# Kernel optimization log

Measured on AMD Instinct MI355X. Metric: run time of the kernel, lower is better.

Reference implementation:

```python
import jax, jax.numpy as jnp
import numpy as np

B, S, D_MODEL, D_HEAD = 8, 2048, 1024, 128
MAX_ROUNDS = 3
THRESH = 0.1
SCALE = 1.0 / np.sqrt(float(D_HEAD))


def setup_inputs() -> dict:
    key = jax.random.key(0)
    ks = jax.random.split(key, 12)

    def lin(k, out_d, in_d):
        # torch Linear weight layout [out, in], y = x @ W.T + b
        return (jax.random.normal(k, (out_d, in_d), jnp.float32) / np.sqrt(float(in_d))).astype(jnp.float32)

    thesis_w = lin(ks[3], D_HEAD, D_HEAD)
    return {
        "x": jax.random.normal(ks[0], (B, S, D_MODEL), jnp.float32),
        "wq": lin(ks[1], D_HEAD, D_MODEL),
        "wk": lin(ks[2], D_HEAD, D_MODEL),
        "wv": lin(ks[4], D_HEAD, D_MODEL),
        "thesis_w": thesis_w,  # antithesis weight is -thesis_w per __init__
        "thesis_b": 0.02 * jax.random.normal(ks[5], (D_HEAD,), jnp.float32),
        "anti_b": 0.02 * jax.random.normal(ks[6], (D_HEAD,), jnp.float32),
        "s_w1": lin(ks[7], D_HEAD, 3 * D_HEAD),
        "s_b1": jnp.zeros((D_HEAD,), jnp.float32),
        "s_w2": lin(ks[8], D_HEAD, D_HEAD),
        "s_b2": jnp.zeros((D_HEAD,), jnp.float32),
        "g_w": lin(ks[9], 1, 2 * D_HEAD),
        "g_b": jnp.zeros((1,), jnp.float32),
    }


def reference(x, wq, wk, wv, thesis_w, thesis_b, anti_b, s_w1, s_b1, s_w2, s_b2, g_w, g_b):
    # q/k/v projections (no bias)
    q = jnp.einsum("bsm,hm->bsh", x, wq)
    k = jnp.einsum("bsm,hm->bsh", x, wk)
    v = jnp.einsum("bsm,hm->bsh", x, wv)

    attn = jax.nn.softmax(jnp.einsum("bqh,bkh->bqk", q, k) * SCALE, axis=-1)
    # dropout is identity at eval time
    cur = jnp.einsum("bqk,bkh->bqh", attn, v)  # [B,S,Dh]

    # attn_weights and v never change across rounds, so thesis/antithesis are
    # round-invariant: compute the context projections once.
    context = cur
    thesis = context @ thesis_w.T + thesis_b
    anti = context @ (-thesis_w).T + anti_b  # antithesis weight = -thesis weight

    active = jnp.ones((B, S), dtype=bool)
    for _ in range(MAX_ROUNDS):
        # emulate `if not active_mask.any(): break` under jit
        any_active = jnp.any(active)
        am = active[..., None].astype(x.dtype)
        at, aa, ac = thesis * am, anti * am, cur * am

        h = jax.nn.relu(jnp.concatenate([at, aa, ac], axis=-1) @ s_w1.T + s_b1)
        synth = h @ s_w2.T + s_b2
        gate = jax.nn.sigmoid(jnp.concatenate([ac, synth], axis=-1) @ g_w.T + g_b)
        update = gate * (synth - ac) * 0.1
        new = cur + update  # applied to ALL tokens, matching original

        stable = jnp.linalg.norm(update, axis=-1) < THRESH  # new - cur == update
        cur = jnp.where(any_active, new, cur)
        active = jnp.where(any_active, active & ~stable, active)
    return cur
```

## Files before the change

### kernel.cpp

```cpp
#include <hip/hip_runtime.h>
#include <hip/hip_bf16.h>

#define B_   8
#define S_   2048
#define DM   1024
#define DH   128
#define BS_  16384
#define SCALE_  0.08838834764831845f
#define SCALE2_ 0.12751744f

typedef unsigned short u16;
typedef unsigned int   u32;
typedef _Float16 half8 __attribute__((ext_vector_type(8)));
typedef __bf16   bf16x8 __attribute__((ext_vector_type(8)));
typedef float    f32x4 __attribute__((ext_vector_type(4)));
typedef u32      u32x4 __attribute__((ext_vector_type(4)));

union H8 { u32x4 v; u32 u[4]; half8 h; bf16x8 b; };

__device__ __forceinline__ float bf2f(u16 u) {
    union { u32 i; float f; } w; w.i = ((u32)u) << 16; return w.f;
}
__device__ __forceinline__ void unpack8(uint4 v, float* f) {
    f[0] = bf2f(v.x & 0xffff); f[1] = bf2f(v.x >> 16);
    f[2] = bf2f(v.y & 0xffff); f[3] = bf2f(v.y >> 16);
    f[4] = bf2f(v.z & 0xffff); f[5] = bf2f(v.z >> 16);
    f[6] = bf2f(v.w & 0xffff); f[7] = bf2f(v.w >> 16);
}
__device__ __forceinline__ float ldE(const void* b, size_t i, int isbf16) {
    return isbf16 ? bf2f(((const u16*)b)[i]) : ((const float*)b)[i];
}
__device__ __forceinline__ void ld8(const void* b, size_t i, int isbf16, float* f) {
    if (isbf16) {
        unpack8(*(const uint4*)((const u16*)b + i), f);
    } else {
        float4 a = *(const float4*)((const float*)b + i);
        float4 c = *(const float4*)((const float*)b + i + 4);
        f[0] = a.x; f[1] = a.y; f[2] = a.z; f[3] = a.w;
        f[4] = c.x; f[5] = c.y; f[6] = c.z; f[7] = c.w;
    }
}
__device__ __forceinline__ u32 f2pk(float v) {
    _Float16 h = (_Float16)v;
    _Float16 l = (_Float16)(v - (float)h);
    union { _Float16 f; u16 u; } a, b; a.f = h; b.f = l;
    return ((u32)a.u << 16) | (u32)b.u;
}
__device__ __forceinline__ void split8(const float* f, u32x4& hi, u32x4& lo) {
    u32 H[8], L[8];
#pragma unroll
    for (int j = 0; j < 8; ++j) {
        _Float16 h = (_Float16)f[j];
        _Float16 l = (_Float16)(f[j] - (float)h);
        union { _Float16 x; u16 u; } a, b; a.x = h; b.x = l;
        H[j] = a.u; L[j] = b.u;
    }
    hi = (u32x4){H[0] | (H[1] << 16), H[2] | (H[3] << 16), H[4] | (H[5] << 16), H[6] | (H[7] << 16)};
    lo = (u32x4){L[0] | (L[1] << 16), L[2] | (L[3] << 16), L[4] | (L[5] << 16), L[6] | (L[7] << 16)};
}
__device__ __forceinline__ u32 permHI(u32 eB, u32 eA) { return __builtin_amdgcn_perm(eB, eA, 0x07060302u); }
__device__ __forceinline__ u16 f2h(float v) { union { _Float16 f; u16 u; } a; a.f = (_Float16)v; return a.u; }
__device__ __forceinline__ float h2f(u16 u) { union { _Float16 f; u16 u; } a; a.u = u; return (float)a.f; }

__global__ void init_kernel(const void* x, int* flag, int* active, int* counts) {
    int i = blockIdx.x * 256 + threadIdx.x;
    if (i < BS_) active[i] = 1;
    if (i < 4) counts[i] = (i == 0) ? BS_ : 0;
    if (i == 0) {
        const u16* w = (const u16*)x;
        int sane = 0;
        for (int t = 0; t < 256; ++t) {
            int e = (w[2 * t] >> 7) & 0xFF;
            if (e >= 100 && e <= 135) ++sane;
        }
        *flag = (sane >= 192) ? 1 : 0;
    }
}

__global__ __launch_bounds__(256) void prepack_w_kernel(
    const void* __restrict__ wq, const void* __restrict__ wk, const void* __restrict__ wv,
    const int* __restrict__ flag, u32x4* __restrict__ wpk)
{
    const int isb = *flag;
    const int gid = blockIdx.x * 256 + threadIdx.x;
    const int l  = gid & 63;
    const int t  = (gid >> 6) & 7;
    const int ks = (gid >> 9) & 31;
    const int z  = gid >> 14;
    const void* W = (z == 0) ? wq : (z == 1) ? wk : wv;
    const int row = 16 * t + (l & 15);
    const int k0  = ks * 32 + 8 * (l >> 4);
    const size_t base = ((((size_t)z * 32 + ks) * 16) + 2 * t) * 64 + l;
    if (isb) {
        uint4 v = *(const uint4*)((const u16*)W + (size_t)row * DM + k0);
        wpk[base] = (u32x4){v.x, v.y, v.z, v.w};
    } else {
        float f[8];
        ld8(W, (size_t)row * DM + k0, 0, f);
        u32x4 hi, lo;
        split8(f, hi, lo);
        wpk[base]      = hi;
        wpk[base + 64] = lo;
    }
}

__global__ __launch_bounds__(256) void qkv_kernel(
    const void* __restrict__ x, const u32x4* __restrict__ wpk,
    const int* __restrict__ flag, u32* __restrict__ qout,
    u32x4* __restrict__ kfrag, u32x4* __restrict__ vfrag)
{
    const int isb = *flag;
    const int z = blockIdx.z;
    const int bx = blockIdx.x;
    const int m0 = ((bx & 7) * 32 + (bx >> 3)) * 64;
    const int tid = threadIdx.x;
    const int wave = tid >> 6, lane = tid & 63;
    const int qd = lane >> 4, c = lane & 15;

    __shared__ u32x4 WLraw[2][16][64];
    u32x4 (*WLb)[2][8][64] = (u32x4(*)[2][8][64])WLraw;
    u32x4 (*WLf)[8][2][64] = (u32x4(*)[8][2][64])WLraw;
    u16 (*TS)[136] = (u16(*)[136])WLraw;

    const u32x4* wz = wpk + (size_t)z * (32 * 16 * 64);
    const size_t arow = (size_t)(m0 + wave * 16 + c) * DM + 8 * qd;

#define STAGE2(i_, b_)                                                            \
    {                                                                             \
        _Pragma("unroll")                                                         \
        for (int _j = 0; _j < 4; ++_j) {                                          \
            const int _g = wave * 4 + _j, _ksub = _g >> 3, _t = _g & 7;           \
            __builtin_amdgcn_global_load_lds(                                     \
                (const __attribute__((address_space(1))) u32*)(                   \
                    wz + ((size_t)(2 * (i_) + _ksub) * 16 + 2 * _t) * 64 + lane), \
                (__attribute__((address_space(3))) u32*)&WLb[b_][_ksub][_t][0],   \
                16, 0, 0);                                                        \
        }                                                                         \
    }
#define STAGE_W(ks_, b_)                                                          \
    {                                                                             \
        const u32x4* _src = wz + ((size_t)(ks_) * 16 + 4 * wave) * 64 + lane;     \
        _Pragma("unroll")                                                         \
        for (int _j = 0; _j < 4; ++_j) {                                          \
            __builtin_amdgcn_global_load_lds(                                     \
                (const __attribute__((address_space(1))) u32*)(_src + _j * 64),   \
                (__attribute__((address_space(3))) u32*)&WLf[b_][2 * wave + (_j >> 1)][_j & 1][0], \
                16, 0, 0);                                                        \
        }                                                                         \
    }

    f32x4 acc[8] = {};

    if (isb) {
        const u16* xb = (const u16*)x;
        uint4 A0 = *(const uint4*)(xb + arow);
        uint4 A1 = *(const uint4*)(xb + arow + 32);
        STAGE2(0, 0);
        uint4 A0n = *(const uint4*)(xb + arow + 64);
        uint4 A1n = *(const uint4*)(xb + arow + 96);
        __syncthreads();
        for (int i = 0; i < 16; ++i) {
            const int cb = i & 1;
            if (i + 1 < 16) STAGE2(i + 1, cb ^ 1);
            H8 Ah0; Ah0.v = (u32x4){A0.x, A0.y, A0.z, A0.w};
            H8 Ah1; Ah1.v = (u32x4){A1.x, A1.y, A1.z, A1.w};
#pragma unroll
            for (int t = 0; t < 8; ++t) {
                H8 bh; bh.v = WLb[cb][0][t][lane];
                acc[t] = __builtin_amdgcn_mfma_f32_16x16x32_bf16(Ah0.b, bh.b, acc[t], 0, 0, 0);
            }
#pragma unroll
            for (int t = 0; t < 8; ++t) {
                H8 bh; bh.v = WLb[cb][1][t][lane];
                acc[t] = __builtin_amdgcn_mfma_f32_16x16x32_bf16(Ah1.b, bh.b, acc[t], 0, 0, 0);
            }
            A0 = A0n; A1 = A1n;
            if (i + 2 < 16) {
                A0n = *(const uint4*)(xb + arow + (size_t)(i + 2) * 64);
                A1n = *(const uint4*)(xb + arow + (size_t)(i + 2) * 64 + 32);
            }
            __syncthreads();
        }
    } else {
        float Ar[8], Arn[8];
        ld8(x, arow, 0, Ar);
        STAGE_W(0, 0);
        ld8(x, arow + 32, 0, Arn);
        __syncthreads();
        for (int ks = 0; ks < 32; ++ks) {
            const int cb = ks & 1;
            if (ks + 1 < 32) STAGE_W(ks + 1, cb ^ 1);
            H8 Ah, Al;
            split8(Ar, Ah.v, Al.v);
#pragma unroll
            for (int t = 0; t < 8; ++t) {
                H8 bh, bl;
                bh.v = WLf[cb][t][0][lane]; bl.v = WLf[cb][t][1][lane];
                acc[t] = __builtin_amdgcn_mfma_f32_16x16x32_f16(Al.h, bh.h, acc[t], 0, 0, 0);
                acc[t] = __builtin_amdgcn_mfma_f32_16x16x32_f16(Ah.h, bl.h, acc[t], 0, 0, 0);
                acc[t] = __builtin_amdgcn_mfma_f32_16x16x32_f16(Ah.h, bh.h, acc[t], 0, 0, 0);
            }
#pragma unroll
            for (int j = 0; j < 8; ++j) Ar[j] = Arn[j];
            if (ks + 2 < 32) ld8(x, arow + (size_t)(ks + 2) * 32, 0, Arn);
            __syncthreads();
        }
    }
#undef STAGE2
#undef STAGE_W

    if (z == 0) {
#pragma unroll
        for (int r = 0; r < 4; ++r) {
            const int row = m0 + wave * 16 + qd * 4 + r;
            u32* op = qout + (size_t)row * DH + c;
#pragma unroll
            for (int t = 0; t < 8; ++t) op[t * 16] = f2pk(acc[t][r]);
        }
    } else {
#pragma unroll
        for (int t = 0; t < 8; ++t)
#pragma unroll
            for (int r = 0; r < 4; ++r)
                TS[wave * 16 + qd * 4 + r][16 * t + c] = f2h(acc[t][r]);
        __syncthreads();
        if (z == 1) {
#pragma unroll
            for (int i = 0; i < 4; ++i) {
                const int f = tid + 256 * i;
                const int lf = f & 63, ks = (f >> 6) & 3, sub = f >> 8;
                const int key = sub * 16 + (lf & 15);
                const int d0  = ks * 32 + 8 * (lf >> 4);
                u32 w[4];
#pragma unroll
                for (int q = 0; q < 4; ++q)
                    w[q] = (u32)TS[key][d0 + 2 * q] | ((u32)TS[key][d0 + 2 * q + 1] << 16);
                kfrag[((size_t)(m0 / 16 + sub) * 4 + ks) * 64 + lf] = (u32x4){w[0], w[1], w[2], w[3]};
            }
        } else {
#pragma unroll
            for (int i = 0; i < 4; ++i) {
                const int f = tid + 256 * i;
                const int lf = f & 63, t = (f >> 6) & 7, sub = f >> 9;
                const int kb2 = sub * 32 + 8 * (lf >> 4);
                const int dh  = 16 * t + (lf & 15);
                u32 w[4];
#pragma unroll
                for (int q = 0; q < 4; ++q)
                    w[q] = (u32)TS[kb2 + 2 * q][dh] | ((u32)TS[kb2 + 2 * q + 1][dh] << 16);
                vfrag[((size_t)(m0 / 32 + sub) * 8 + t) * 64 + lf] = (u32x4){w[0], w[1], w[2], w[3]};
            }
        }
    }
}

template <bool WRITE_PARTIAL>
__device__ __forceinline__ void attn_body(
    const u32* qp, const u32x4* __restrict__ kfrag, const u32x4* __restrict__ vfrag,
    u16* outO, u16* outL, float* cur,
    int b, int q0, int kt0, int kt1, int part)
{
    const int tid = threadIdx.x;
    const int wave = tid >> 6, lane = tid & 63;
    const int qd = lane >> 4, c = lane & 15;

    __shared__ u16 PB[4][531];

    H8 Qh[4];
    {
        const u32* qr = qp + ((size_t)b * S_ + q0 + wave * 16 + c) * DH;
#pragma unroll
        for (int ks = 0; ks < 4; ++ks) {
            uint4 e0 = *(const uint4*)(qr + ks * 32 + qd * 8);
            uint4 e1 = *(const uint4*)(qr + ks * 32 + qd * 8 + 4);
            Qh[ks].u[0] = permHI(e0.y, e0.x); Qh[ks].u[1] = permHI(e0.w, e0.z);
            Qh[ks].u[2] = permHI(e1.y, e1.x); Qh[ks].u[3] = permHI(e1.w, e1.z);
        }
    }

    f32x4 O[8] = {};
    float lsum[4] = {};

    const u32x4* kb0 = kfrag + (size_t)b * 128 * 256;
    const u32x4* vb0 = vfrag + (size_t)b * 64 * 512;

    for (int kt = kt0; kt < kt1; ++kt) {
        const u32x4* kf = kb0 + (size_t)kt * 512;
        const u32x4* vf = vb0 + (size_t)kt * 512;

        f32x4 S0 = {}, S1 = {};
#pragma unroll
        for (int ks = 0; ks < 4; ++ks) {
            H8 kh;
            kh.v = kf[ks * 64 + lane];
            S0 = __builtin_amdgcn_mfma_f32_16x16x32_f16(Qh[ks].h, kh.h, S0, 0, 0, 0);
            kh.v = kf[256 + ks * 64 + lane];
            S1 = __builtin_amdgcn_mfma_f32_16x16x32_f16(Qh[ks].h, kh.h, S1, 0, 0, 0);
        }

        u16* pw = PB[wave];
#pragma unroll
        for (int r = 0; r < 4; ++r) {
            float e0 = exp2f(fmaf(S0[r], SCALE2_, -4.0f));
            float e1 = exp2f(fmaf(S1[r], SCALE2_, -4.0f));
            lsum[r] += e0 + e1;
            pw[(4 * qd + r) * 33 + c]      = f2h(e0);
            pw[(4 * qd + r) * 33 + 16 + c] = f2h(e1);
        }

        u16 e[8];
#pragma unroll
        for (int j = 0; j < 8; ++j) e[j] = pw[c * 33 + 8 * qd + j];
        H8 Ph;
        Ph.u[0] = (u32)e[0] | ((u32)e[1] << 16);
        Ph.u[1] = (u32)e[2] | ((u32)e[3] << 16);
        Ph.u[2] = (u32)e[4] | ((u32)e[5] << 16);
        Ph.u[3] = (u32)e[6] | ((u32)e[7] << 16);

#pragma unroll
        for (int t = 0; t < 8; ++t) {
            H8 vh;
            vh.v = vf[t * 64 + lane];
            O[t] = __builtin_amdgcn_mfma_f32_16x16x32_f16(Ph.h, vh.h, O[t], 0, 0, 0);
        }
    }

    if (WRITE_PARTIAL) {
        float lred[4];
#pragma unroll
        for (int r = 0; r < 4; ++r) {
            float l = lsum[r];
            l += __shfl_xor(l, 1); l += __shfl_xor(l, 2);
            l += __shfl_xor(l, 4); l += __shfl_xor(l, 8);
            lred[r] = l;
        }
        const size_t rb = (size_t)b * S_ + q0 + wave * 16 + 4 * qd;
        u16* Op = outO + (size_t)part * ((size_t)BS_ * DH);
#pragma unroll
        for (int t = 0; t < 8; ++t)
#pragma unroll
            for (int r = 0; r < 4; ++r)
                Op[(rb + r) * DH + t * 16 + c] = f2h(O[t][r]);
        if (c == 0) {
            u16* lp = outL + (size_t)part * BS_;
#pragma unroll
            for (int r = 0; r < 4; ++r) lp[rb + r] = f2h(lred[r]);
        }
    } else {
        float linv[4];
#pragma unroll
        for (int r = 0; r < 4; ++r) {
            float l = lsum[r];
            l += __shfl_xor(l, 1); l += __shfl_xor(l, 2);
            l += __shfl_xor(l, 4); l += __shfl_xor(l, 8);
            linv[r] = 1.0f / l;
        }
        const size_t rb = (size_t)b * S_ + q0 + wave * 16 + 4 * qd;
#pragma unroll
        for (int t = 0; t < 8; ++t)
#pragma unroll
            for (int r = 0; r < 4; ++r)
                cur[(rb + r) * DH + t * 16 + c] = O[t][r] * linv[r];
    }
}

__global__ __launch_bounds__(256) void attn_kernel(
    const u32* qp, const u32x4* __restrict__ kfrag, const u32x4* __restrict__ vfrag, float* cur)
{
    const int rid = blockIdx.x + 32 * blockIdx.y;
    attn_body<false>(qp, kfrag, vfrag, nullptr, nullptr, cur,
                     rid & 7, ((rid >> 3) & 31) * 64, 0, S_ / 32, 0);
}

__global__ __launch_bounds__(256) void attn_split_kernel(
    const u32* qp, const u32x4* __restrict__ kfrag, const u32x4* __restrict__ vfrag,
    u16* __restrict__ Opart, u16* __restrict__ lpart)
{
    const int rid = blockIdx.x + 32 * (blockIdx.y + 8 * blockIdx.z);
    const int b    = rid & 7;
    const int qx   = (rid >> 3) & 31;
    const int part = rid >> 8;
    const int quart = S_ / 128;
    attn_body<true>(qp, kfrag, vfrag, Opart, lpart, nullptr,
                    b, qx * 64, part * quart, (part + 1) * quart, part);
}

__global__ __launch_bounds__(256) void combine_kernel(
    const u16* __restrict__ Opart, const u16* __restrict__ lpart,
    float* __restrict__ cur)
{
    const size_t N1 = (size_t)BS_ * DH;
    const size_t i0 = ((size_t)blockIdx.x * 256 + threadIdx.x) * 16;
    const int row = (int)(i0 >> 7);
    const float lt = h2f(lpart[row]) + h2f(lpart[BS_ + row])
                   + h2f(lpart[2 * BS_ + row]) + h2f(lpart[3 * BS_ + row]);
    const float linv = 1.0f / lt;
    float acc[16] = {};
#pragma unroll
    for (int p = 0; p < 4; ++p) {
        const u16* op = Opart + (size_t)p * N1 + i0;
        uint4 v0 = *(const uint4*)op;
        uint4 v1 = *(const uint4*)(op + 8);
        const u32 w[8] = {v0.x, v0.y, v0.z, v0.w, v1.x, v1.y, v1.z, v1.w};
#pragma unroll
        for (int j = 0; j < 8; ++j) {
            acc[2 * j]     += h2f((u16)(w[j] & 0xffff));
            acc[2 * j + 1] += h2f((u16)(w[j] >> 16));
        }
    }
#pragma unroll
    for (int t = 0; t < 4; ++t)
        *(float4*)(cur + i0 + t * 4) = make_float4(
            acc[4*t] * linv, acc[4*t+1] * linv, acc[4*t+2] * linv, acc[4*t+3] * linv);
}

__global__ __launch_bounds__(256) void prepack_rw_kernel(
    const void* __restrict__ tw, const void* __restrict__ w1, const void* __restrict__ w2,
    const int* __restrict__ flag, u32x4* __restrict__ pk)
{
    const int isb = *flag;
    const int gid = blockIdx.x * 256 + threadIdx.x;
    const int l = gid & 63, t = (gid >> 6) & 7, ks = (gid >> 9) & 3, mat = gid >> 11;
    const int row = 16 * t + (l & 15);
    const int k0  = ks * 32 + 8 * (l >> 4);
    float f[8];
    if (mat == 0)      ld8(tw, (size_t)row * DH + k0, isb, f);
    else if (mat <= 3) ld8(w1, (size_t)row * 384 + (mat - 1) * 128 + k0, isb, f);
    else               ld8(w2, (size_t)row * DH + k0, isb, f);
    u32x4 hi, lo;
    split8(f, hi, lo);
    const size_t base = (((size_t)mat * 4 + ks) * 16 + 2 * t) * 64 + l;
    pk[base] = hi; pk[base + 64] = lo;
}

struct Afrag { H8 h[4], l[4]; };
__device__ __forceinline__ void splitA(const float (&A)[4][8], Afrag& F) {
#pragma unroll
    for (int ks = 0; ks < 4; ++ks) split8(A[ks], F.h[ks].v, F.l[ks].v);
}

__global__ __launch_bounds__(256) void round_kernel(
    const float* cur0, const float* curr,
    const u32x4* __restrict__ pk,
    const void* __restrict__ tb, const void* __restrict__ ab,
    const void* __restrict__ b1, const void* __restrict__ b2,
    const void* __restrict__ gw, const void* __restrict__ gb,
    const int* __restrict__ flag, int* active, int* counts, int r,
    float* cur_out, void* dout)
{
    const int isb = *flag;
    const int tok0 = blockIdx.x * 64;
    const int tid = threadIdx.x;
    const bool last = (dout != nullptr);

    if (counts[r] <= 0) {
        if (last) {
            for (int e = tid; e < 64 * DH; e += 256) {
                size_t idx = (size_t)tok0 * DH + e;
                float v = curr[idx];
                if (isb) ((__hip_bfloat16*)dout)[idx] = __float2bfloat16(v);
                else     ((float*)dout)[idx] = v;
            }
        }
        return;
    }

    const int wave = tid >> 6, lane = tid & 63;
    const int qd = lane >> 4, c = lane & 15;

    __shared__ u32x4 WB[4][8][64];
    __shared__ u16 T0S[64][132];
    __shared__ u16 HSS[64][132];
    __shared__ float actS[64], tbS[128], abS[128], b1S[128], b2S[128], gwS[256];
    __shared__ int blkcnt;

    auto stageB = [&](int mat) {
#pragma unroll
        for (int j = 0; j < 8; ++j) {
            __builtin_amdgcn_global_load_lds(
                (const __attribute__((address_space(1))) u32*)(
                    pk + (((size_t)mat * 4 + wave) * 16 + 2 * j) * 64 + lane),
                (__attribute__((address_space(3))) u32*)&WB[wave][j][0],
                16, 0, 0);
        }
    };
    auto stageF = [&](int mat, int h) {
#pragma unroll
        for (int j = 0; j < 8; ++j) {
            const int g = wave * 8 + j, kl = g >> 4, p = (g >> 3) & 1, t = g & 7;
            __builtin_amdgcn_global_load_lds(
                (const __attribute__((address_space(1))) u32*)(
                    pk + (((size_t)mat * 4 + 2 * h + kl) * 16 + 2 * t + p) * 64 + lane),
                (__attribute__((address_space(3))) u32*)&WB[kl * 2 + p][t][0],
                16, 0, 0);
        }
    };
    auto gemmB = [&](const Afrag& F, f32x4 (&acc)[8]) {
#pragma unroll
        for (int ks = 0; ks < 4; ++ks)
#pragma unroll
            for (int t = 0; t < 8; ++t) {
                H8 bh; bh.v = WB[ks][t][lane];
                acc[t] = __builtin_amdgcn_mfma_f32_16x16x32_f16(F.l[ks].h, bh.h, acc[t], 0, 0, 0);
                acc[t] = __builtin_amdgcn_mfma_f32_16x16x32_f16(F.h[ks].h, bh.h, acc[t], 0, 0, 0);
            }
    };
    auto gemmF = [&](const Afrag& F, int h, f32x4 (&acc)[8]) {
#pragma unroll
        for (int kl = 0; kl < 2; ++kl) {
            const int ks = 2 * h + kl;
#pragma unroll
            for (int t = 0; t < 8; ++t) {
                H8 bh, bl;
                bh.v = WB[kl * 2][t][lane];
                bl.v = WB[kl * 2 + 1][t][lane];
                acc[t] = __builtin_amdgcn_mfma_f32_16x16x32_f16(F.l[ks].h, bh.h, acc[t], 0, 0, 0);
                acc[t] = __builtin_amdgcn_mfma_f32_16x16x32_f16(F.h[ks].h, bl.h, acc[t], 0, 0, 0);
                acc[t] = __builtin_amdgcn_mfma_f32_16x16x32_f16(F.h[ks].h, bh.h, acc[t], 0, 0, 0);
            }
        }
    };
    auto runGemm = [&](int mat, const Afrag& F, f32x4 (&acc)[8]) {
        if (isb) {
            gemmB(F, acc);
        } else {
            gemmF(F, 0, acc);
            __syncthreads();
            stageF(mat, 1);
            __syncthreads();
            gemmF(F, 1, acc);
        }
    };

    if (isb) stageB(0); else stageF(0, 0);
    if (tid < 64) actS[tid] = active[tok0 + tid] ? 1.0f : 0.0f;
    if (tid < 128) {
        tbS[tid] = ldE(tb, tid, isb); abS[tid] = ldE(ab, tid, isb);
        b1S[tid] = ldE(b1, tid, isb); b2S[tid] = ldE(b2, tid, isb);
    }
    gwS[tid] = ldE(gw, tid, isb);
    if (tid == 0) blkcnt = 0;
    const float gbf = ldE(gb, 0, isb);

    const int rowl = 16 * wave + c;
    const int hr   = 16 * wave + 4 * qd;

    float A1[4][8];
    {
        const float* cr = cur0 + (size_t)(tok0 + rowl) * DH;
#pragma unroll
        for (int ks = 0; ks < 4; ++ks) {
            *(float4*)&A1[ks][0] = *(const float4*)(cr + ks * 32 + 8 * qd);
            *(float4*)&A1[ks][4] = *(const float4*)(cr + ks * 32 + 8 * qd + 4);
        }
    }
    Afrag FA; splitA(A1, FA);
    __syncthreads();

    {
        f32x4 acc[8] = {};
        runGemm(0, FA, acc);
#pragma unroll
        for (int t = 0; t < 8; ++t)
#pragma unroll
            for (int rr = 0; rr < 4; ++rr)
                T0S[hr + rr][16 * t + c] = f2h(acc[t][rr]);
    }
    __syncthreads();
    if (isb) stageB(1); else stageF(1, 0);

    f32x4 acc1[8] = {};
    const float am_r = actS[rowl];
    {
        float Ac[4][8];
#pragma unroll
        for (int ks = 0; ks < 4; ++ks)
#pragma unroll
            for (int j = 0; j < 8; ++j) {
                const int k = ks * 32 + 8 * qd + j;
                Ac[ks][j] = (h2f(T0S[rowl][k]) + tbS[k]) * am_r;
            }
        Afrag FC; splitA(Ac, FC);
        __syncthreads();
        runGemm(1, FC, acc1);
    }
    __syncthreads();
    if (isb) stageB(2); else stageF(2, 0);
    {
        float Ac[4][8];
#pragma unroll
        for (int ks = 0; ks < 4; ++ks)
#pragma unroll
            for (int j = 0; j < 8; ++j) {
                const int k = ks * 32 + 8 * qd + j;
                Ac[ks][j] = (abS[k] - h2f(T0S[rowl][k])) * am_r;
            }
        Afrag FC; splitA(Ac, FC);
        __syncthreads();
        runGemm(2, FC, acc1);
    }
    __syncthreads();
    if (isb) stageB(3); else stageF(3, 0);
    {
        float Ac[4][8];
        const float* cr = curr + (size_t)(tok0 + rowl) * DH;
#pragma unroll
        for (int ks = 0; ks < 4; ++ks) {
            float4 a0 = *(const float4*)(cr + ks * 32 + 8 * qd);
            float4 a1 = *(const float4*)(cr + ks * 32 + 8 * qd + 4);
            Ac[ks][0] = a0.x * am_r; Ac[ks][1] = a0.y * am_r;
            Ac[ks][2] = a0.z * am_r; Ac[ks][3] = a0.w * am_r;
            Ac[ks][4] = a1.x * am_r; Ac[ks][5] = a1.y * am_r;
            Ac[ks][6] = a1.z * am_r; Ac[ks][7] = a1.w * am_r;
        }
        Afrag FC; splitA(Ac, FC);
        __syncthreads();
        runGemm(3, FC, acc1);
    }
#pragma unroll
    for (int t = 0; t < 8; ++t)
#pragma unroll
        for (int rr = 0; rr < 4; ++rr)
            HSS[hr + rr][16 * t + c] = f2h(fmaxf(acc1[t][rr] + b1S[16 * t + c], 0.0f));
    __syncthreads();
    if (isb) stageB(4); else stageF(4, 0);
    {
        float Ac[4][8];
#pragma unroll
        for (int ks = 0; ks < 4; ++ks)
#pragma unroll
            for (int j = 0; j < 8; ++j)
                Ac[ks][j] = h2f(HSS[rowl][ks * 32 + 8 * qd + j]);
        Afrag FC; splitA(Ac, FC);
        __syncthreads();
        f32x4 acc2[8] = {};
        runGemm(4, FC, acc2);
#pragma unroll
        for (int t = 0; t < 8; ++t)
#pragma unroll
            for (int rr = 0; rr < 4; ++rr)
                T0S[hr + rr][16 * t + c] = f2h(acc2[t][rr] + b2S[16 * t + c]);
    }
    __syncthreads();

    const int tok = tid >> 2, d0 = (tid & 3) * 32;
    const float am = actS[tok];
    const float* cp = curr + (size_t)(tok0 + tok) * DH + d0;
    float cv[32];
#pragma unroll
    for (int t = 0; t < 8; ++t) {
        float4 vv = *(const float4*)(cp + t * 4);
        cv[t * 4] = vv.x; cv[t * 4 + 1] = vv.y; cv[t * 4 + 2] = vv.z; cv[t * 4 + 3] = vv.w;
    }
    float srow[32];
#pragma unroll
    for (int e = 0; e < 32; ++e) srow[e] = h2f(T0S[tok][d0 + e]);
    float gp = 0.0f;
#pragma unroll
    for (int e = 0; e < 32; ++e)
        gp += cv[e] * am * gwS[d0 + e] + srow[e] * gwS[128 + d0 + e];
    gp += __shfl_xor(gp, 1, 4);
    gp += __shfl_xor(gp, 2, 4);
    const float gate = 1.0f / (1.0f + __expf(-(gp + gbf)));
    float ss = 0.0f; float up[32];
#pragma unroll
    for (int e = 0; e < 32; ++e) {
        float u = gate * (srow[e] - cv[e] * am) * 0.1f;
        up[e] = u; ss += u * u;
    }
    ss += __shfl_xor(ss, 1, 4);
    ss += __shfl_xor(ss, 2, 4);
    const bool stable = sqrtf(ss) < 0.1f;

    if (last) {
        size_t off = (size_t)(tok0 + tok) * DH + d0;
        if (isb) {
            __hip_bfloat16* op = (__hip_bfloat16*)dout + off;
#pragma unroll
            for (int e = 0; e < 32; ++e) op[e] = __float2bfloat16(cv[e] + up[e]);
        } else {
            float* op = (float*)dout + off;
#pragma unroll
            for (int t = 0; t < 8; ++t)
                *(float4*)(op + t * 4) = make_float4(cv[t * 4] + up[t * 4], cv[t * 4 + 1] + up[t * 4 + 1],
                                                     cv[t * 4 + 2] + up[t * 4 + 2], cv[t * 4 + 3] + up[t * 4 + 3]);
        }
    } else {
        float* op = cur_out + (size_t)(tok0 + tok) * DH + d0;
#pragma unroll
        for (int t = 0; t < 8; ++t)
            *(float4*)(op + t * 4) = make_float4(cv[t * 4] + up[t * 4], cv[t * 4 + 1] + up[t * 4 + 1],
                                                 cv[t * 4 + 2] + up[t * 4 + 2], cv[t * 4 + 3] + up[t * 4 + 3]);
    }
    const int newact = (am > 0.0f && !stable) ? 1 : 0;
    if ((tid & 3) == 0) {
        active[tok0 + tok] = newact;
        if (newact) atomicAdd(&blkcnt, 1);
    }
    __syncthreads();
    if (tid == 0 && blkcnt > 0) atomicAdd(&counts[r + 1], blkcnt);
}

extern "C" void kernel_launch(void* const* d_in, const int* in_sizes, int n_in,
                              void* d_out, int out_size, void* d_ws, size_t ws_size,
                              hipStream_t stream) {
    const void* x  = d_in[0];
    const void* wq = d_in[1];
    const void* wk = d_in[2];
    const void* wv = d_in[3];
    const void* tw = d_in[4];
    const void* tb = d_in[5];
    const void* ab = d_in[6];
    const void* w1 = d_in[7];
    const void* b1 = d_in[8];
    const void* w2 = d_in[9];
    const void* b2 = d_in[10];
    const void* gw = d_in[11];
    const void* gb = d_in[12];

    u32* ws = (u32*)d_ws;
    const size_t N1 = (size_t)BS_ * DH;
    u32* qp = ws;
    u32* kp = ws + N1;
    u32* vp = ws + 2 * N1;
    int* active = (int*)(ws + 3 * N1);
    int* counts = active + BS_;
    int* flag   = counts + 4;
    float* cur0  = (float*)qp;
    float* cur_r = (float*)kp;
    u16* Opart16 = (u16*)(ws + 3 * N1 + 32768);
    u16* lpart16 = (u16*)(ws + 5 * N1 + 32768);
    const bool big_ws = ws_size >= (size_t)42300000;
    u32x4* wpk = (u32x4*)(ws + 3 * N1 + 32768);
    u32x4* pkRW = (u32x4*)vp;
    u32x4* kfragP = (u32x4*)kp;
    u32x4* vfragP = (u32x4*)vp;

    init_kernel<<<dim3(BS_ / 256), 256, 0, stream>>>(x, flag, active, counts);
    prepack_w_kernel<<<dim3(192), 256, 0, stream>>>(wq, wk, wv, flag, wpk);
    qkv_kernel<<<dim3(BS_ / 64, 1, 3), 256, 0, stream>>>(x, wpk, flag, qp, kfragP, vfragP);
    if (big_ws) {
        attn_split_kernel<<<dim3(S_ / 64, B_, 4), 256, 0, stream>>>(qp, kfragP, vfragP, Opart16, lpart16);
        combine_kernel<<<dim3(512), 256, 0, stream>>>(Opart16, lpart16, cur0);
    } else {
        attn_kernel<<<dim3(S_ / 64, B_), 256, 0, stream>>>(qp, kfragP, vfragP, cur0);
    }
    prepack_rw_kernel<<<dim3(40), 256, 0, stream>>>(tw, w1, w2, flag, pkRW);
    round_kernel<<<dim3(BS_ / 64), 256, 0, stream>>>(
        cur0, cur0, pkRW, tb, ab, b1, b2, gw, gb, flag, active, counts, 0, cur_r, nullptr);
    round_kernel<<<dim3(BS_ / 64), 256, 0, stream>>>(
        cur0, cur_r, pkRW, tb, ab, b1, b2, gw, gb, flag, active, counts, 1, cur_r, nullptr);
    round_kernel<<<dim3(BS_ / 64), 256, 0, stream>>>(
        cur0, cur_r, pkRW, tb, ab, b1, b2, gw, gb, flag, active, counts, 2, cur_r, d_out);
}
```

Measured before the change: 261.3 us.

## Halve round-kernel token tile, split N across waves, double-buffer weight staging

The round kernel now processes 32 tokens per block instead of 64, with waves arranged as 2 row groups by 2 column halves, so each wave computes 4 output tiles rather than 8. Weight staging into LDS is double-buffered, so the next matrix's load is issued before the current GEMM runs, and several barriers are removed. T0S and HSS are merged into one shared buffer. The aim is more blocks for better occupancy and to overlap weight fetches with MFMA work. In exchange, each weight matrix is fetched twice as often across the grid and per-block fixed overhead grows.

```diff
diff --git a/kernel.cpp b/kernel.cpp
--- a/kernel.cpp
+++ b/kernel.cpp
@@ -449,13 +449,13 @@
     float* cur_out, void* dout)
 {
     const int isb = *flag;
-    const int tok0 = blockIdx.x * 64;
+    const int tok0 = blockIdx.x * 32;
     const int tid = threadIdx.x;
     const bool last = (dout != nullptr);
 
     if (counts[r] <= 0) {
         if (last) {
-            for (int e = tid; e < 64 * DH; e += 256) {
+            for (int e = tid; e < 32 * DH; e += 256) {
                 size_t idx = (size_t)tok0 * DH + e;
                 float v = curr[idx];
                 if (isb) ((__hip_bfloat16*)dout)[idx] = __float2bfloat16(v);
@@ -467,73 +467,75 @@
 
     const int wave = tid >> 6, lane = tid & 63;
     const int qd = lane >> 4, c = lane & 15;
-
-    __shared__ u32x4 WB[4][8][64];
-    __shared__ u16 T0S[64][132];
-    __shared__ u16 HSS[64][132];
-    __shared__ float actS[64], tbS[128], abS[128], b1S[128], b2S[128], gwS[256];
+    const int rowg = wave >> 1, colh = wave & 1;
+
+    __shared__ u32x4 WB[2][4][8][64];
+    __shared__ u16 TS[32][132];
+    __shared__ float actS[32], tbS[128], abS[128], b1S[128], b2S[128], gwS[256];
     __shared__ int blkcnt;
 
-    auto stageB = [&](int mat) {
+    auto stageB = [&](int mat, int buf) {
 #pragma unroll
         for (int j = 0; j < 8; ++j) {
+            const int g = wave * 8 + j, ks = g >> 3, t = g & 7;
             __builtin_amdgcn_global_load_lds(
                 (const __attribute__((address_space(1))) u32*)(
-                    pk + (((size_t)mat * 4 + wave) * 16 + 2 * j) * 64 + lane),
-                (__attribute__((address_space(3))) u32*)&WB[wave][j][0],
+                    pk + (((size_t)mat * 4 + ks) * 16 + 2 * t) * 64 + lane),
+                (__attribute__((address_space(3))) u32*)&WB[buf][ks][t][0],
                 16, 0, 0);
         }
     };
-    auto stageF = [&](int mat, int h) {
+    auto stageF = [&](int mat, int h, int buf) {
 #pragma unroll
         for (int j = 0; j < 8; ++j) {
             const int g = wave * 8 + j, kl = g >> 4, p = (g >> 3) & 1, t = g & 7;
             __builtin_amdgcn_global_load_lds(
                 (const __attribute__((address_space(1))) u32*)(
                     pk + (((size_t)mat * 4 + 2 * h + kl) * 16 + 2 * t + p) * 64 + lane),
-                (__attribute__((address_space(3))) u32*)&WB[kl * 2 + p][t][0],
+                (__attribute__((address_space(3))) u32*)&WB[buf][kl * 2 + p][t][0],
                 16, 0, 0);
         }
     };
-    auto gemmB = [&](const Afrag& F, f32x4 (&acc)[8]) {
+    auto gemmB = [&](const Afrag& F, int buf, f32x4 (&acc)[4]) {
 #pragma unroll
         for (int ks = 0; ks < 4; ++ks)
 #pragma unroll
-            for (int t = 0; t < 8; ++t) {
-                H8 bh; bh.v = WB[ks][t][lane];
-                acc[t] = __builtin_amdgcn_mfma_f32_16x16x32_f16(F.l[ks].h, bh.h, acc[t], 0, 0, 0);
-                acc[t] = __builtin_amdgcn_mfma_f32_16x16x32_f16(F.h[ks].h, bh.h, acc[t], 0, 0, 0);
+            for (int tl = 0; tl < 4; ++tl) {
+                H8 bh; bh.v = WB[buf][ks][4 * colh + tl][lane];
+                acc[tl] = __builtin_amdgcn_mfma_f32_16x16x32_f16(F.l[ks].h, bh.h, acc[tl], 0, 0, 0);
+                acc[tl] = __builtin_amdgcn_mfma_f32_16x16x32_f16(F.h[ks].h, bh.h, acc[tl], 0, 0, 0);
             }
     };
-    auto gemmF = [&](const Afrag& F, int h, f32x4 (&acc)[8]) {
+    auto gemmFh = [&](const Afrag& F, int h, int buf, f32x4 (&acc)[4]) {
 #pragma unroll
         for (int kl = 0; kl < 2; ++kl) {
             const int ks = 2 * h + kl;
 #pragma unroll
-            for (int t = 0; t < 8; ++t) {
+            for (int tl = 0; tl < 4; ++tl) {
                 H8 bh, bl;
-                bh.v = WB[kl * 2][t][lane];
-                bl.v = WB[kl * 2 + 1][t][lane];
-                acc[t] = __builtin_amdgcn_mfma_f32_16x16x32_f16(F.l[ks].h, bh.h, acc[t], 0, 0, 0);
-                acc[t] = __builtin_amdgcn_mfma_f32_16x16x32_f16(F.h[ks].h, bl.h, acc[t], 0, 0, 0);
-                acc[t] = __builtin_amdgcn_mfma_f32_16x16x32_f16(F.h[ks].h, bh.h, acc[t], 0, 0, 0);
+                bh.v = WB[buf][kl * 2][4 * colh + tl][lane];
+                bl.v = WB[buf][kl * 2 + 1][4 * colh + tl][lane];
+                acc[tl] = __builtin_amdgcn_mfma_f32_16x16x32_f16(F.l[ks].h, bh.h, acc[tl], 0, 0, 0);
+                acc[tl] = __builtin_amdgcn_mfma_f32_16x16x32_f16(F.h[ks].h, bl.h, acc[tl], 0, 0, 0);
+                acc[tl] = __builtin_amdgcn_mfma_f32_16x16x32_f16(F.h[ks].h, bh.h, acc[tl], 0, 0, 0);
             }
         }
     };
-    auto runGemm = [&](int mat, const Afrag& F, f32x4 (&acc)[8]) {
+    auto STAGE = [&](int mat, int buf) { if (isb) stageB(mat, buf); else stageF(mat, 0, buf); };
+    auto GEMM = [&](int mat, const Afrag& F, int buf, f32x4 (&acc)[4]) {
         if (isb) {
-            gemmB(F, acc);
+            gemmB(F, buf, acc);
         } else {
-            gemmF(F, 0, acc);
+            gemmFh(F, 0, buf, acc);
             __syncthreads();
-            stageF(mat, 1);
+            stageF(mat, 1, buf);
             __syncthreads();
-            gemmF(F, 1, acc);
+            gemmFh(F, 1, buf, acc);
         }
     };
 
-    if (isb) stageB(0); else stageF(0, 0);
-    if (tid < 64) actS[tid] = active[tok0 + tid] ? 1.0f : 0.0f;
+    STAGE(0, 0);
+    if (tid < 32) actS[tid] = active[tok0 + tid] ? 1.0f : 0.0f;
     if (tid < 128) {
         tbS[tid] = ldE(tb, tid, isb); abS[tid] = ldE(ab, tid, isb);
         b1S[tid] = ldE(b1, tid, isb); b2S[tid] = ldE(b2, tid, isb);
@@ -542,8 +544,8 @@
     if (tid == 0) blkcnt = 0;
     const float gbf = ldE(gb, 0, isb);
 
-    const int rowl = 16 * wave + c;
-    const int hr   = 16 * wave + 4 * qd;
+    const int rowl = 16 * rowg + c;
+    const int hr   = 16 * rowg + 4 * qd;
 
     float A1[4][8];
     {
@@ -557,19 +559,20 @@
     Afrag FA; splitA(A1, FA);
     __syncthreads();
 
+    STAGE(1, 1);
     {
-        f32x4 acc[8] = {};
-        runGemm(0, FA, acc);
-#pragma unroll
-        for (int t = 0; t < 8; ++t)
+        f32x4 accT[4] = {};
+        GEMM(0, FA, 0, accT);
+#pragma unroll
+        for (int tl = 0; tl < 4; ++tl)
 #pragma unroll
             for (int rr = 0; rr < 4; ++rr)
-                T0S[hr + rr][16 * t + c] = f2h(acc[t][rr]);
+                TS[hr + rr][16 * (4 * colh + tl) + c] = f2h(accT[tl][rr]);
     }
     __syncthreads();
-    if (isb) stageB(1); else stageF(1, 0);
-
-    f32x4 acc1[8] = {};
+
+    STAGE(2, 0);
+    f32x4 acc1[4] = {};
     const float am_r = actS[rowl];
     {
         float Ac[4][8];
@@ -578,14 +581,14 @@
 #pragma unroll
             for (int j = 0; j < 8; ++j) {
                 const int k = ks * 32 + 8 * qd + j;
-                Ac[ks][j] = (h2f(T0S[rowl][k]) + tbS[k]) * am_r;
+                Ac[ks][j] = (h2f(TS[rowl][k]) + tbS[k]) * am_r;
             }
         Afrag FC; splitA(Ac, FC);
-        __syncthreads();
-        runGemm(1, FC, acc1);
+        GEMM(1, FC, 1, acc1);
     }
     __syncthreads();
-    if (isb) stageB(2); else stageF(2, 0);
+
+    STAGE(3, 1);
     {
         float Ac[4][8];
 #pragma unroll
@@ -593,14 +596,14 @@
 #pragma unroll
             for (int j = 0; j < 8; ++j) {
                 const int k = ks * 32 + 8 * qd + j;
-                Ac[ks][j] = (abS[k] - h2f(T0S[rowl][k])) * am_r;
+                Ac[ks][j] = (abS[k] - h2f(TS[rowl][k])) * am_r;
             }
         Afrag FC; splitA(Ac, FC);
-        __syncthreads();
-        runGemm(2, FC, acc1);
+        GEMM(2, FC, 0, acc1);
     }
     __syncthreads();
-    if (isb) stageB(3); else stageF(3, 0);
+
+    STAGE(4, 0);
     {
         float Ac[4][8];
         const float* cr = curr + (size_t)(tok0 + rowl) * DH;
@@ -614,62 +617,67 @@
             Ac[ks][6] = a1.z * am_r; Ac[ks][7] = a1.w * am_r;
         }
         Afrag FC; splitA(Ac, FC);
-        __syncthreads();
-        runGemm(3, FC, acc1);
-    }
-#pragma unroll
-    for (int t = 0; t < 8; ++t)
-#pragma unroll
-        for (int rr = 0; rr < 4; ++rr)
-            HSS[hr + rr][16 * t + c] = f2h(fmaxf(acc1[t][rr] + b1S[16 * t + c], 0.0f));
+        GEMM(3, FC, 1, acc1);
+    }
+#pragma unroll
+    for (int tl = 0; tl < 4; ++tl)
+#pragma unroll
+        for (int rr = 0; rr < 4; ++rr) {
+            const int col = 16 * (4 * colh + tl) + c;
+            TS[hr + rr][col] = f2h(fmaxf(acc1[tl][rr] + b1S[col], 0.0f));
+        }
     __syncthreads();
-    if (isb) stageB(4); else stageF(4, 0);
+
     {
         float Ac[4][8];
 #pragma unroll
         for (int ks = 0; ks < 4; ++ks)
 #pragma unroll
             for (int j = 0; j < 8; ++j)
-                Ac[ks][j] = h2f(HSS[rowl][ks * 32 + 8 * qd + j]);
+                Ac[ks][j] = h2f(TS[rowl][ks * 32 + 8 * qd + j]);
         Afrag FC; splitA(Ac, FC);
+        f32x4 acc2[4] = {};
+        GEMM(4, FC, 0, acc2);
         __syncthreads();
-        f32x4 acc2[8] = {};
-        runGemm(4, FC, acc2);
-#pragma unroll
-        for (int t = 0; t < 8; ++t)
-#pragma unroll
-            for (int rr = 0; rr < 4; ++rr)
-                T0S[hr + rr][16 * t + c] = f2h(acc2[t][rr] + b2S[16 * t + c]);
+#pragma unroll
+        for (int tl = 0; tl < 4; ++tl)
+#pragma unroll
+            for (int rr = 0; rr < 4; ++rr) {
+                const int col = 16 * (4 * colh + tl) + c;
+                TS[hr + rr][col] = f2h(acc2[tl][rr] + b2S[col]);
+            }
     }
     __syncthreads();
 
-    const int tok = tid >> 2, d0 = (tid & 3) * 32;
+    const int tok = tid >> 3, d0 = (tid & 7) * 16;
     const float am = actS[tok];
     const float* cp = curr + (size_t)(tok0 + tok) * DH + d0;
-    float cv[32];
-#pragma unroll
-    for (int t = 0; t < 8; ++t) {
+    float cv[16];
+#pragma unroll
+    for (int t = 0; t < 4; ++t) {
         float4 vv = *(const float4*)(cp + t * 4);
         cv[t * 4] = vv.x; cv[t * 4 + 1] = vv.y; cv[t * 4 + 2] = vv.z; cv[t * 4 + 3] = vv.w;
     }
-    float srow[32];
-#pragma unroll
-    for (int e = 0; e < 32; ++e) srow[e] = h2f(T0S[tok][d0 + e]);
+    float srow[16];
+#pragma unroll
+    for (int e = 0; e < 16; ++e) srow[e] = h2f(TS[tok][d0 + e]);
     float gp = 0.0f;
 #pragma unroll
-    for (int e = 0; e < 32; ++e)
+    for (int e = 0; e < 16; ++e)
         gp += cv[e] * am * gwS[d0 + e] + srow[e] * gwS[128 + d0 + e];
-    gp += __shfl_xor(gp, 1, 4);
-    gp += __shfl_xor(gp, 2, 4);
+    gp += __shfl_xor(gp, 1, 8);
+    gp += __shfl_xor(gp, 2, 8);
+    gp += __shfl_xor(gp, 4, 8);
     const float gate = 1.0f / (1.0f + __expf(-(gp + gbf)));
-    float ss = 0.0f; float up[32];
-#pragma unroll
-    for (int e = 0; e < 32; ++e) {
+    float ss = 0.0f; float up[16];
+#pragma unroll
+    for (int e = 0; e < 16; ++e) {
         float u = gate * (srow[e] - cv[e] * am) * 0.1f;
         up[e] = u; ss += u * u;
     }
-    ss += __shfl_xor(ss, 1, 4);
-    ss += __shfl_xor(ss, 2, 4);
+    ss += __shfl_xor(ss, 1, 8);
+    ss += __shfl_xor(ss, 2, 8);
+    ss += __shfl_xor(ss, 4, 8);
     const bool stable = sqrtf(ss) < 0.1f;
 
     if (last) {
@@ -677,23 +685,23 @@
         if (isb) {
             __hip_bfloat16* op = (__hip_bfloat16*)dout + off;
 #pragma unroll
-            for (int e = 0; e < 32; ++e) op[e] = __float2bfloat16(cv[e] + up[e]);
+            for (int e = 0; e < 16; ++e) op[e] = __float2bfloat16(cv[e] + up[e]);
         } else {
             float* op = (float*)dout + off;
 #pragma unroll
-            for (int t = 0; t < 8; ++t)
+            for (int t = 0; t < 4; ++t)
                 *(float4*)(op + t * 4) = make_float4(cv[t * 4] + up[t * 4], cv[t * 4 + 1] + up[t * 4 + 1],
                                                      cv[t * 4 + 2] + up[t * 4 + 2], cv[t * 4 + 3] + up[t * 4 + 3]);
         }
     } else {
         float* op = cur_out + (size_t)(tok0 + tok) * DH + d0;
 #pragma unroll
-        for (int t = 0; t < 8; ++t)
+        for (int t = 0; t < 4; ++t)
             *(float4*)(op + t * 4) = make_float4(cv[t * 4] + up[t * 4], cv[t * 4 + 1] + up[t * 4 + 1],
                                                  cv[t * 4 + 2] + up[t * 4 + 2], cv[t * 4 + 3] + up[t * 4 + 3]);
     }
     const int newact = (am > 0.0f && !stable) ? 1 : 0;
-    if ((tid & 3) == 0) {
+    if ((tid & 7) == 0) {
         active[tok0 + tok] = newact;
         if (newact) atomicAdd(&blkcnt, 1);
     }
@@ -746,10 +754,10 @@
         attn_kernel<<<dim3(S_ / 64, B_), 256, 0, stream>>>(qp, kfragP, vfragP, cur0);
     }
     prepack_rw_kernel<<<dim3(40), 256, 0, stream>>>(tw, w1, w2, flag, pkRW);
-    round_kernel<<<dim3(BS_ / 64), 256, 0, stream>>>(
+    round_kernel<<<dim3(BS_ / 32), 256, 0, stream>>>(
         cur0, cur0, pkRW, tb, ab, b1, b2, gw, gb, flag, active, counts, 0, cur_r, nullptr);
-    round_kernel<<<dim3(BS_ / 64), 256, 0, stream>>>(
+    round_kernel<<<dim3(BS_ / 32), 256, 0, stream>>>(
         cur0, cur_r, pkRW, tb, ab, b1, b2, gw, gb, flag, active, counts, 1, cur_r, nullptr);
-    round_kernel<<<dim3(BS_ / 64), 256, 0, stream>>>(
+    round_kernel<<<dim3(BS_ / 32), 256, 0, stream>>>(
         cur0, cur_r, pkRW, tb, ab, b1, b2, gw, gb, flag, active, counts, 2, cur_r, d_out);
 }
```

Result: no change. 256.5 us, median of 2 (-1.9%).
